# Optimization experiments

Hardware: AMD Instinct MI355X
Metric: run time of the kernel (lower is better)

## Reference

```python
import jax, jax.numpy as jnp
import numpy as np

T, B, H, V = 128, 32, 1024, 32000


def setup_inputs() -> dict:
    key = jax.random.key(0)
    ks = jax.random.split(key, 8)
    scale = 1.0 / np.sqrt(H)
    return {
        "input": jax.random.normal(ks[0], (T, B, H), dtype=jnp.float32),
        "hidden": jnp.zeros((B, H), dtype=jnp.float32),
        "w_ic": jax.random.uniform(ks[1], (H, H), jnp.float32, -scale, scale),
        "w_ix": jax.random.uniform(ks[2], (H, H), jnp.float32, -scale, scale),
        "w_fc": jax.random.uniform(ks[3], (H, H), jnp.float32, -scale, scale),
        "w_fx": jax.random.uniform(ks[4], (H, H), jnp.float32, -scale, scale),
        "b_i": jnp.zeros((H,), dtype=jnp.float32),
        "b_f": jnp.zeros((H,), dtype=jnp.float32),
        "W_out": jax.random.uniform(ks[5], (V, H), jnp.float32, -scale, scale),
        "b_out": jnp.zeros((V,), dtype=jnp.float32),
    }


def reference(input, hidden, w_ic, w_ix, w_fc, w_fx, b_i, b_f, W_out, b_out):
    # Precompute input projections for all timesteps: [T, B, H]
    ix = jnp.einsum("tbh,kh->tbk", input, w_ix)
    fx = jnp.einsum("tbh,kh->tbk", input, w_fx)

    def step(c, xs):
        ix_t, fx_t, x_t = xs
        i_t = jax.nn.sigmoid(c @ w_ic.T + b_i + ix_t)
        f_t = jax.nn.sigmoid(c @ w_fc.T + b_f + fx_t)
        c_new = i_t * x_t + f_t * c  # RAN gated-additive update
        return c_new, c_new

    hidden_final, outputs = jax.lax.scan(step, hidden, (ix, fx, input))
    logits = jnp.einsum("tbh,vh->tbv", outputs, W_out) + b_out
    log_probs = jax.nn.log_softmax(logits, axis=-1)
    return log_probs, hidden_final
```

## Files before the change

kernel.cpp:

```cpp
#include <hip/hip_runtime.h>

typedef __attribute__((ext_vector_type(4))) float f32x4;
typedef __attribute__((ext_vector_type(8))) short bf16x8;
typedef __attribute__((ext_vector_type(4))) unsigned u32x4;

#define T_DIM 128
#define B_DIM 32
#define H_DIM 1024
#define V_DIM 32000
#define MROWS 4096
#define NBLK 64
#define PUBSTEP 32768
#define WSTRIDE 1028
#define GBK 32

__device__ __forceinline__ ushort f2bf(float f){
  union { float f; unsigned u; } x; x.f = f;
  unsigned u = x.u;
  unsigned r = (u + 0x7fffu + ((u >> 16) & 1u)) >> 16;
  return (ushort)r;
}
__device__ __forceinline__ float bf2f(ushort h){
  union { unsigned u; float f; } x; x.u = ((unsigned)h) << 16;
  return x.f;
}

__device__ __forceinline__ void async_copy16(void* lds, const void* g){
  __builtin_amdgcn_global_load_lds((const __attribute__((address_space(1))) void*)g,
                                   (__attribute__((address_space(3))) void*)lds, 16, 0, 0);
}

__global__ void cast_bf16_kernel(const float* __restrict__ s, ushort* __restrict__ d, int n4){
  int stride = gridDim.x * blockDim.x;
  for (int i = blockIdx.x*blockDim.x + threadIdx.x; i < n4; i += stride){
    float4 v = ((const float4*)s)[i];
    ushort4 o = make_ushort4(f2bf(v.x), f2bf(v.y), f2bf(v.z), f2bf(v.w));
    ((ushort4*)d)[i] = o;
  }
}

__global__ void cast_split_kernel(const float* __restrict__ s, ushort* __restrict__ dh,
                                  ushort* __restrict__ dl, int n4){
  int stride = gridDim.x * blockDim.x;
  for (int i = blockIdx.x*blockDim.x + threadIdx.x; i < n4; i += stride){
    float4 v = ((const float4*)s)[i];
    ushort4 h = make_ushort4(f2bf(v.x), f2bf(v.y), f2bf(v.z), f2bf(v.w));
    ushort4 l = make_ushort4(f2bf(v.x - bf2f(h.x)), f2bf(v.y - bf2f(h.y)),
                             f2bf(v.z - bf2f(h.z)), f2bf(v.w - bf2f(h.w)));
    ((ushort4*)dh)[i] = h;
    ((ushort4*)dl)[i] = l;
  }
}

__global__ __launch_bounds__(256) void gemm_bt_plain(
    const ushort* __restrict__ A, const ushort* __restrict__ B,
    float* __restrict__ C, int N, int K, int NTN)
{
  __shared__ ushort lA[128*32];
  __shared__ ushort lB[128*32];
  int tid = threadIdx.x;
  int lane = tid & 63, wid = tid >> 6;
  int tm = blockIdx.x / NTN, tn = blockIdx.x % NTN;
  int row0 = tm << 7, col0 = tn << 7;

  f32x4 acc[4][4] = {};

  auto stage = [&](const ushort* __restrict__ g, ushort* l, int r0, int k0){
    int c = wid << 1;
    const ushort* s0 = g + (size_t)(r0 + (c<<4) + (lane>>2))*K + k0 + ((lane&3)<<3);
    async_copy16(l + (c<<9), s0);
    async_copy16(l + ((c+1)<<9), s0 + (size_t)16*K);
  };

  int nk = K >> 5;
  stage(A, lA, row0, 0);
  stage(B, lB, col0, 0);
  int wm = (wid >> 1) << 6, wn = (wid & 1) << 6;
  int kg = (lane >> 4) << 3;
  int ar = lane & 15;

  for (int kt = 0; kt < nk; ++kt){
    __syncthreads();
    bf16x8 af[4], bfr[4];
    #pragma unroll
    for (int mi = 0; mi < 4; ++mi) af[mi]  = *(const bf16x8*)&lA[(wm + mi*16 + ar)*32 + kg];
    #pragma unroll
    for (int ni = 0; ni < 4; ++ni) bfr[ni] = *(const bf16x8*)&lB[(wn + ni*16 + ar)*32 + kg];
    #pragma unroll
    for (int mi = 0; mi < 4; ++mi)
      #pragma unroll
      for (int ni = 0; ni < 4; ++ni)
        acc[mi][ni] = __builtin_amdgcn_mfma_f32_16x16x32_bf16(af[mi], bfr[ni], acc[mi][ni], 0, 0, 0);
    if (kt + 1 < nk){
      __syncthreads();
      stage(A, lA, row0, (kt+1) << 5);
      stage(B, lB, col0, (kt+1) << 5);
    }
  }

  int rr = (lane >> 4) << 2;
  #pragma unroll
  for (int mi = 0; mi < 4; ++mi)
    #pragma unroll
    for (int ni = 0; ni < 4; ++ni){
      int r  = row0 + wm + mi*16 + rr;
      int cc = col0 + wn + ni*16 + ar;
      #pragma unroll
      for (int q = 0; q < 4; ++q)
        C[(size_t)(r + q) * N + cc] = acc[mi][ni][q];
    }
}

__global__ __launch_bounds__(512) void gemm256(
    const ushort* __restrict__ A, const ushort* __restrict__ B,
    float* __restrict__ C, const float* __restrict__ bias,
    float* __restrict__ pmax, float* __restrict__ psum)
{
  __shared__ ushort lA[4][256*GBK];
  __shared__ ushort lB[4][256*GBK];
  __shared__ float redm[2][4][128], reds[2][4][128];

  const int K = 1024, N = V_DIM, NTN = 125, NT = 32;
  int tid = threadIdx.x, lane = tid & 63, wid = tid >> 6;
  int wm = wid >> 2, wn = wid & 3;
  int bid = blockIdx.x;
  int xcd = bid & 7, id = bid >> 3;
  int tm = (xcd << 1) | (id & 1);
  int tn = id >> 1;
  int row0 = tm << 8, col0 = tn << 8;
  int ar = lane & 15, kg = (lane >> 4) << 3;

  auto STAGE = [&](int slot, int kt){
    int k0 = kt << 5;
    #pragma unroll
    for (int j = 0; j < 2; ++j){
      int u = j*512 + tid;
      int r = u >> 2, p = u & 3;
      int g = p ^ ((r >> 1) & 3);
      int rA = row0 + r, k = k0 + (g << 3);
      const ushort* sA = A + ((size_t)(rA>>5)<<15) + ((size_t)(k>>4)<<9) + ((rA&31)<<4) + (k&15);
      async_copy16(&lA[slot][u<<3], sA);
    }
    #pragma unroll
    for (int j = 0; j < 2; ++j){
      int u = j*512 + tid;
      int r = u >> 2, p = u & 3;
      int g = p ^ ((r >> 1) & 3);
      const ushort* sB = B + (size_t)(col0 + r)*K + k0 + (g << 3);
      async_copy16(&lB[slot][u<<3], sB);
    }
  };

  f32x4 acc[8][4] = {};

  STAGE(0, 0);
  STAGE(1, 1);
  int gk = kg >> 3;
  for (int t = 0; t < NT; ++t){
    if (t + 2 < NT) STAGE((t+2) & 3, t+2);
    if (t + 2 < NT)      asm volatile("s_waitcnt vmcnt(8)" ::: "memory");
    else if (t + 1 < NT) asm volatile("s_waitcnt vmcnt(4)" ::: "memory");
    else                 asm volatile("s_waitcnt vmcnt(0)" ::: "memory");
    __builtin_amdgcn_s_barrier();
    __builtin_amdgcn_sched_barrier(0);
    const ushort* bufA = lA[t & 3];
    const ushort* bufB = lB[t & 3];
    bf16x8 a[8], b[4];
    #pragma unroll
    for (int fr = 0; fr < 8; ++fr){
      int row = wm*128 + fr*16 + ar;
      int phys = gk ^ ((row >> 1) & 3);
      a[fr] = *(const bf16x8*)&bufA[row*GBK + (phys << 3)];
    }
    #pragma unroll
    for (int fc = 0; fc < 4; ++fc){
      int row = wn*64 + fc*16 + ar;
      int phys = gk ^ ((row >> 1) & 3);
      b[fc] = *(const bf16x8*)&bufB[row*GBK + (phys << 3)];
    }
    __builtin_amdgcn_s_setprio(1);
    #pragma unroll
    for (int fr = 0; fr < 8; ++fr)
      #pragma unroll
      for (int fc = 0; fc < 4; ++fc)
        acc[fr][fc] = __builtin_amdgcn_mfma_f32_16x16x32_bf16(a[fr], b[fc], acc[fr][fc], 0, 0, 0);
    __builtin_amdgcn_s_setprio(0);
    __builtin_amdgcn_sched_barrier(0);
  }

  float bb4[4];
  #pragma unroll
  for (int fc = 0; fc < 4; ++fc) bb4[fc] = bias[col0 + wn*64 + fc*16 + ar];
  #pragma unroll
  for (int fr = 0; fr < 8; ++fr){
    #pragma unroll
    for (int q = 0; q < 4; ++q){
      int rl = fr*16 + (lane>>4)*4 + q;
      int r = row0 + wm*128 + rl;
      float vals[4];
      #pragma unroll
      for (int fc = 0; fc < 4; ++fc){
        vals[fc] = acc[fr][fc][q] + bb4[fc];
        C[(size_t)r * N + col0 + wn*64 + fc*16 + ar] = vals[fc];
      }
      float m = fmaxf(fmaxf(vals[0], vals[1]), fmaxf(vals[2], vals[3]));
      #pragma unroll
      for (int o = 1; o < 16; o <<= 1) m = fmaxf(m, __shfl_xor(m, o));
      float s = expf(vals[0]-m) + expf(vals[1]-m) + expf(vals[2]-m) + expf(vals[3]-m);
      #pragma unroll
      for (int o = 1; o < 16; o <<= 1) s += __shfl_xor(s, o);
      if (ar == 0){ redm[wm][wn][rl] = m; reds[wm][wn][rl] = s; }
    }
  }
  __syncthreads();
  if (tid < 256){
    int wm2 = tid >> 7, rl = tid & 127;
    float m0 = redm[wm2][0][rl], m1 = redm[wm2][1][rl];
    float m2 = redm[wm2][2][rl], m3 = redm[wm2][3][rl];
    float M = fmaxf(fmaxf(m0, m1), fmaxf(m2, m3));
    float S = reds[wm2][0][rl]*expf(m0-M) + reds[wm2][1][rl]*expf(m1-M)
            + reds[wm2][2][rl]*expf(m2-M) + reds[wm2][3][rl]*expf(m3-M);
    int r = row0 + wm2*128 + rl;
    pmax[(size_t)r*NTN + tn] = M;
    psum[(size_t)r*NTN + tn] = S;
  }
}

__global__ __launch_bounds__(512) void ran_all(
    unsigned* __restrict__ pub, ushort* __restrict__ cst,
    const float* __restrict__ hiddenf,
    const ushort* __restrict__ wh, const ushort* __restrict__ wl,
    const float* __restrict__ b_i, const float* __restrict__ b_f,
    const float* __restrict__ ixfx, const float* __restrict__ x_all,
    float* __restrict__ hid_final)
{
  __shared__ ushort lWh[32*WSTRIDE];
  __shared__ ushort lWl[32*WSTRIDE];
  __shared__ f32x4 part[4][2][2][64];
  __shared__ float gsm[2*32*17];
  __shared__ float cfl[32][17];

  int tid = threadIdx.x, lane = tid & 63, wid = tid >> 6;
  int kq = wid & 3, mh = wid >> 2;
  int rgate = wid & 1, rmh = (wid >> 1) & 1;
  int bid = blockIdx.x;
  int nb = bid << 4;
  int ar = lane & 15, kg = (lane >> 4) << 3;
  int um = tid >> 4, uk = tid & 15;

  #pragma unroll
  for (int u = 0; u < 8; ++u){
    int unit = u*512 + tid;
    int r = unit >> 7, off = (unit & 127) << 3;
    int g = r >> 4, c = r & 15;
    size_t gsrc = (size_t)((g<<10) + nb + c) * H_DIM + off;
    *(bf16x8*)&lWh[r*WSTRIDE + off] = *(const bf16x8*)&wh[gsrc];
    *(bf16x8*)&lWl[r*WSTRIDE + off] = *(const bf16x8*)&wl[gsrc];
  }
  cfl[um][uk] = hiddenf[(um<<10) + nb + uk];
  float bb = (rgate ? b_f : b_i)[nb + ar];
  const ushort* b0h = &lWh[(     ar)*WSTRIDE + (kq<<8) + kg];
  const ushort* b0l = &lWl[(     ar)*WSTRIDE + (kq<<8) + kg];
  const ushort* b1h = &lWh[(16 + ar)*WSTRIDE + (kq<<8) + kg];
  const ushort* b1l = &lWl[(16 + ar)*WSTRIDE + (kq<<8) + kg];
  int abase = (kq<<13) + ((kg>>4)<<9) + (((mh<<4) + ar)<<4) + (kg & 8);
  __syncthreads();

  for (int t = 0; t < T_DIM; ++t){
    float xq1 = x_all[((size_t)t<<15) + (um<<10) + nb + uk];
    float pix[4];
    if (wid < 4){
      const float* ix_t = ixfx + ((size_t)t<<16);
      #pragma unroll
      for (int q = 0; q < 4; ++q){
        int m = (rmh<<4) + ((lane>>4)<<2) + q;
        pix[q] = ix_t[m*2048 + (rgate<<10) + nb + ar];
      }
    }

    const unsigned* ps = pub + ((size_t)t << 15) + abase;
    unsigned expt = (unsigned)(t + 1) << 16;
    u32x4 w0[8], w1[8];
    int tries = 0;
    while (1){
      #pragma unroll
      for (int f = 0; f < 8; ++f){
        const unsigned* p = ps + (f << 10);
        asm volatile("global_load_dwordx4 %0, %2, off sc0 sc1\n\t"
                     "global_load_dwordx4 %1, %2, off offset:16 sc0 sc1"
                     : "=&v"(w0[f]), "=&v"(w1[f]) : "v"(p));
      }
      asm volatile("s_waitcnt vmcnt(0)" ::: "memory");
      __builtin_amdgcn_sched_barrier(0);
      unsigned bad = 0;
      #pragma unroll
      for (int f = 0; f < 8; ++f){
        bad |= (w0[f][0]^expt)|(w0[f][1]^expt)|(w0[f][2]^expt)|(w0[f][3]^expt)
             | (w1[f][0]^expt)|(w1[f][1]^expt)|(w1[f][2]^expt)|(w1[f][3]^expt);
      }
      if (__ballot((bad & 0xFFFF0000u) != 0) == 0ull) break;
      if (++tries > (1<<15)) break;
    }

    f32x4 g0h = {}, g0l = {}, g1h = {}, g1l = {};
    #pragma unroll
    for (int f = 0; f < 8; ++f){
      union { unsigned u[4]; bf16x8 v; } cv;
      cv.u[0] = (w0[f][0] & 0xFFFFu) | (w0[f][1] << 16);
      cv.u[1] = (w0[f][2] & 0xFFFFu) | (w0[f][3] << 16);
      cv.u[2] = (w1[f][0] & 0xFFFFu) | (w1[f][1] << 16);
      cv.u[3] = (w1[f][2] & 0xFFFFu) | (w1[f][3] << 16);
      int ob = f << 5;
      bf16x8 v0h = *(const bf16x8*)&b0h[ob];
      bf16x8 v0l = *(const bf16x8*)&b0l[ob];
      bf16x8 v1h = *(const bf16x8*)&b1h[ob];
      bf16x8 v1l = *(const bf16x8*)&b1l[ob];
      g0h = __builtin_amdgcn_mfma_f32_16x16x32_bf16(cv.v, v0h, g0h, 0, 0, 0);
      g0l = __builtin_amdgcn_mfma_f32_16x16x32_bf16(cv.v, v0l, g0l, 0, 0, 0);
      g1h = __builtin_amdgcn_mfma_f32_16x16x32_bf16(cv.v, v1h, g1h, 0, 0, 0);
      g1l = __builtin_amdgcn_mfma_f32_16x16x32_bf16(cv.v, v1l, g1l, 0, 0, 0);
    }
    part[kq][mh][0][lane] = g0h + g0l;
    part[kq][mh][1][lane] = g1h + g1l;
    __syncthreads();

    if (wid < 4){
      f32x4 sum = part[0][rmh][rgate][lane] + part[1][rmh][rgate][lane]
                + part[2][rmh][rgate][lane] + part[3][rmh][rgate][lane];
      #pragma unroll
      for (int q = 0; q < 4; ++q){
        int m = (rmh<<4) + ((lane>>4)<<2) + q;
        float pre = sum[q] + bb + pix[q];
        gsm[((rgate<<5) + m)*17 + ar] = 1.f / (1.f + expf(-pre));
      }
    }
    __syncthreads();

    {
      float iv = gsm[um*17 + uk];
      float fv = gsm[(32+um)*17 + uk];
      float cv2 = cfl[um][uk];
      float cn = iv * xq1 + fv * cv2;
      cfl[um][uk] = cn;
      ushort hb = f2bf(cn);
      unsigned word = ((unsigned)(t + 2) << 16) | (unsigned)hb;
      __hip_atomic_store(&pub[((size_t)(t+1) << 15) + (bid << 9) + tid], word,
                         __ATOMIC_RELAXED, __HIP_MEMORY_SCOPE_AGENT);
      cst[((size_t)t << 15) + (bid << 9) + tid] = hb;
      if (t == T_DIM-1) hid_final[(um<<10) + nb + uk] = cn;
    }
    __syncthreads();
  }
}

__global__ void init_c_kernel(const float* __restrict__ hidden, unsigned* __restrict__ pub){
  int i = blockIdx.x * blockDim.x + threadIdx.x;
  float v = hidden[i];
  int m = i >> 10, col = i & 1023;
  pub[((col>>4)<<9) + (m<<4) + (col&15)] = (1u << 16) | (unsigned)f2bf(v);
}

__global__ __launch_bounds__(256) void subf_kernel(float* __restrict__ logits,
                                                   const float* __restrict__ pmax,
                                                   const float* __restrict__ psum){
  __shared__ float sl;
  size_t row = blockIdx.x >> 1;
  int half = blockIdx.x & 1;
  int tid = threadIdx.x;
  if (tid < 64){
    float m = -1e30f, s = 0.f;
    for (int i = tid; i < 125; i += 64){
      float mi = pmax[row*125 + i], si = psum[row*125 + i];
      float M = fmaxf(m, mi);
      s = s*expf(m - M) + si*expf(mi - M);
      m = M;
    }
    #pragma unroll
    for (int o = 32; o; o >>= 1){
      float m2 = __shfl_xor(m, o), s2 = __shfl_xor(s, o);
      float M = fmaxf(m, m2);
      s = s*expf(m - M) + s2*expf(m2 - M);
      m = M;
    }
    if (tid == 0) sl = m + logf(s);
  }
  __syncthreads();
  float l = sl;
  float4* p4 = (float4*)(logits + row * (size_t)V_DIM);
  int beg = half * 4000, end = beg + 4000;
  for (int i = beg + tid; i < end; i += 256){
    float4 v = p4[i];
    v.x -= l; v.y -= l; v.z -= l; v.w -= l;
    p4[i] = v;
  }
}

extern "C" void kernel_launch(void* const* d_in, const int* in_sizes, int n_in,
                              void* d_out, int out_size, void* d_ws, size_t ws_size,
                              hipStream_t stream)
{
  const float* input  = (const float*)d_in[0];
  const float* hidden = (const float*)d_in[1];
  const float* w_ic   = (const float*)d_in[2];
  const float* w_ix   = (const float*)d_in[3];
  const float* w_fc   = (const float*)d_in[4];
  const float* w_fx   = (const float*)d_in[5];
  const float* b_i    = (const float*)d_in[6];
  const float* b_f    = (const float*)d_in[7];
  const float* W_out  = (const float*)d_in[8];
  const float* b_out  = (const float*)d_in[9];
  float* out = (float*)d_out;

  char* ws = (char*)d_ws;
  ushort* wout_bf = (ushort*)(ws + 0);
  ushort* in_hi   = (ushort*)(ws + 65536000);
  ushort* wx      = (ushort*)(ws + 73924608);
  ushort* wc_hi   = (ushort*)(ws + 90701824);
  ushort* wc_lo   = (ushort*)(ws + 94896128);
  unsigned* pub   = (unsigned*)(ws + 65536000);
  ushort* cstate  = (ushort*)(ws + 82444288);
  float*  pmax    = (float*)(ws + 94896128);
  float*  psum    = (float*)(ws + 99090432);
  float*  ixfx    = out;

  cast_bf16_kernel<<<2048,256,0,stream>>>(W_out, wout_bf, V_DIM*H_DIM/4);
  cast_bf16_kernel<<<1024,256,0,stream>>>(input, in_hi, MROWS*H_DIM/4);
  cast_bf16_kernel<<<256,256,0,stream>>>(w_ix, wx,             H_DIM*H_DIM/4);
  cast_bf16_kernel<<<256,256,0,stream>>>(w_fx, wx+H_DIM*H_DIM, H_DIM*H_DIM/4);
  cast_split_kernel<<<256,256,0,stream>>>(w_ic, wc_hi,             wc_lo,             H_DIM*H_DIM/4);
  cast_split_kernel<<<256,256,0,stream>>>(w_fc, wc_hi+H_DIM*H_DIM, wc_lo+H_DIM*H_DIM, H_DIM*H_DIM/4);

  gemm_bt_plain<<<32*16,256,0,stream>>>(in_hi, wx, ixfx, 2048, H_DIM, 16);

  hipMemsetAsync(pub, 0, (size_t)129 * PUBSTEP * 4, stream);
  init_c_kernel<<<128,256,0,stream>>>(hidden, pub);

  ran_all<<<NBLK,512,0,stream>>>(pub, cstate, hidden, wc_hi, wc_lo, b_i, b_f,
                                 ixfx, input, out + (size_t)MROWS*V_DIM);

  gemm256<<<2000,512,0,stream>>>(cstate, wout_bf, out, b_out, pmax, psum);
  subf_kernel<<<2*MROWS,256,0,stream>>>(out, pmax, psum);
}
```

Before: 1.867 ms.

## Replace input-projection GEMM with 256x256 multi-buffered swizzled MFMA kernel

Swaps the 128x128 single-buffered input projection GEMM for a 256x256 tile kernel with a 4-slot LDS ring and prefetch two K-steps ahead. LDS tiles use an XOR swizzle, and waits use explicit vmcnt counts instead of full barriers. The aim is to hide global load latency and raise MFMA reuse for the 4096x2048x1024 projection. The trade-off is fewer blocks (128 on a GPU with many CUs), more LDS per block and higher register pressure from 32 accumulator tiles.

Result: no change. 1.863 ms (-0.3%).

```diff
diff --git a/kernel.cpp b/kernel.cpp
--- a/kernel.cpp
+++ b/kernel.cpp
@@ -52,63 +52,86 @@
   }
 }
 
-__global__ __launch_bounds__(256) void gemm_bt_plain(
-    const ushort* __restrict__ A, const ushort* __restrict__ B,
-    float* __restrict__ C, int N, int K, int NTN)
+__global__ __launch_bounds__(512) void gemm256_ix(
+    const ushort* __restrict__ A, const ushort* __restrict__ B, float* __restrict__ C)
 {
-  __shared__ ushort lA[128*32];
-  __shared__ ushort lB[128*32];
-  int tid = threadIdx.x;
-  int lane = tid & 63, wid = tid >> 6;
-  int tm = blockIdx.x / NTN, tn = blockIdx.x % NTN;
-  int row0 = tm << 7, col0 = tn << 7;
-
-  f32x4 acc[4][4] = {};
-
-  auto stage = [&](const ushort* __restrict__ g, ushort* l, int r0, int k0){
-    int c = wid << 1;
-    const ushort* s0 = g + (size_t)(r0 + (c<<4) + (lane>>2))*K + k0 + ((lane&3)<<3);
-    async_copy16(l + (c<<9), s0);
-    async_copy16(l + ((c+1)<<9), s0 + (size_t)16*K);
+  __shared__ ushort lA[4][256*GBK];
+  __shared__ ushort lB[4][256*GBK];
+
+  const int K = 1024, N = 2048, NT = 32;
+  int tid = threadIdx.x, lane = tid & 63, wid = tid >> 6;
+  int wm = wid >> 2, wn = wid & 3;
+  int tn = blockIdx.x & 7, tm = blockIdx.x >> 3;
+  int row0 = tm << 8, col0 = tn << 8;
+  int ar = lane & 15, kg = (lane >> 4) << 3;
+
+  auto STAGE = [&](int slot, int kt){
+    int k0 = kt << 5;
+    #pragma unroll
+    for (int j = 0; j < 2; ++j){
+      int u = j*512 + tid;
+      int r = u >> 2, p = u & 3;
+      int g = p ^ ((r >> 1) & 3);
+      const ushort* sA = A + (size_t)(row0 + r)*K + k0 + (g << 3);
+      async_copy16(&lA[slot][u<<3], sA);
+    }
+    #pragma unroll
+    for (int j = 0; j < 2; ++j){
+      int u = j*512 + tid;
+      int r = u >> 2, p = u & 3;
+      int g = p ^ ((r >> 1) & 3);
+      const ushort* sB = B + (size_t)(col0 + r)*K + k0 + (g << 3);
+      async_copy16(&lB[slot][u<<3], sB);
+    }
   };
 
-  int nk = K >> 5;
-  stage(A, lA, row0, 0);
-  stage(B, lB, col0, 0);
-  int wm = (wid >> 1) << 6, wn = (wid & 1) << 6;
-  int kg = (lane >> 4) << 3;
-  int ar = lane & 15;
-
-  for (int kt = 0; kt < nk; ++kt){
-    __syncthreads();
-    bf16x8 af[4], bfr[4];
-    #pragma unroll
-    for (int mi = 0; mi < 4; ++mi) af[mi]  = *(const bf16x8*)&lA[(wm + mi*16 + ar)*32 + kg];
-    #pragma unroll
-    for (int ni = 0; ni < 4; ++ni) bfr[ni] = *(const bf16x8*)&lB[(wn + ni*16 + ar)*32 + kg];
-    #pragma unroll
-    for (int mi = 0; mi < 4; ++mi)
-      #pragma unroll
-      for (int ni = 0; ni < 4; ++ni)
-        acc[mi][ni] = __builtin_amdgcn_mfma_f32_16x16x32_bf16(af[mi], bfr[ni], acc[mi][ni], 0, 0, 0);
-    if (kt + 1 < nk){
-      __syncthreads();
-      stage(A, lA, row0, (kt+1) << 5);
-      stage(B, lB, col0, (kt+1) << 5);
-    }
-  }
-
-  int rr = (lane >> 4) << 2;
+  f32x4 acc[8][4] = {};
+
+  STAGE(0, 0);
+  STAGE(1, 1);
+  int gk = kg >> 3;
+  for (int t = 0; t < NT; ++t){
+    if (t + 2 < NT) STAGE((t+2) & 3, t+2);
+    if (t + 2 < NT)      asm volatile("s_waitcnt vmcnt(8)" ::: "memory");
+    else if (t + 1 < NT) asm volatile("s_waitcnt vmcnt(4)" ::: "memory");
+    else                 asm volatile("s_waitcnt vmcnt(0)" ::: "memory");
+    __builtin_amdgcn_s_barrier();
+    __builtin_amdgcn_sched_barrier(0);
+    const ushort* bufA = lA[t & 3];
+    const ushort* bufB = lB[t & 3];
+    bf16x8 a[8], b[4];
+    #pragma unroll
+    for (int fr = 0; fr < 8; ++fr){
+      int row = wm*128 + fr*16 + ar;
+      int phys = gk ^ ((row >> 1) & 3);
+      a[fr] = *(const bf16x8*)&bufA[row*GBK + (phys << 3)];
+    }
+    #pragma unroll
+    for (int fc = 0; fc < 4; ++fc){
+      int row = wn*64 + fc*16 + ar;
+      int phys = gk ^ ((row >> 1) & 3);
+      b[fc] = *(const bf16x8*)&bufB[row*GBK + (phys << 3)];
+    }
+    __builtin_amdgcn_s_setprio(1);
+    #pragma unroll
+    for (int fr = 0; fr < 8; ++fr)
+      #pragma unroll
+      for (int fc = 0; fc < 4; ++fc)
+        acc[fr][fc] = __builtin_amdgcn_mfma_f32_16x16x32_bf16(a[fr], b[fc], acc[fr][fc], 0, 0, 0);
+    __builtin_amdgcn_s_setprio(0);
+    __builtin_amdgcn_sched_barrier(0);
+  }
+
   #pragma unroll
-  for (int mi = 0; mi < 4; ++mi)
-    #pragma unroll
-    for (int ni = 0; ni < 4; ++ni){
-      int r  = row0 + wm + mi*16 + rr;
-      int cc = col0 + wn + ni*16 + ar;
-      #pragma unroll
-      for (int q = 0; q < 4; ++q)
-        C[(size_t)(r + q) * N + cc] = acc[mi][ni][q];
-    }
+  for (int fr = 0; fr < 8; ++fr){
+    #pragma unroll
+    for (int q = 0; q < 4; ++q){
+      int r = row0 + wm*128 + fr*16 + (lane>>4)*4 + q;
+      #pragma unroll
+      for (int fc = 0; fc < 4; ++fc)
+        C[(size_t)r * N + col0 + wn*64 + fc*16 + ar] = acc[fr][fc][q];
+    }
+  }
 }
 
 __global__ __launch_bounds__(512) void gemm256(
@@ -430,7 +453,7 @@
   cast_split_kernel<<<256,256,0,stream>>>(w_ic, wc_hi,             wc_lo,             H_DIM*H_DIM/4);
   cast_split_kernel<<<256,256,0,stream>>>(w_fc, wc_hi+H_DIM*H_DIM, wc_lo+H_DIM*H_DIM, H_DIM*H_DIM/4);
 
-  gemm_bt_plain<<<32*16,256,0,stream>>>(in_hi, wx, ixfx, 2048, H_DIM, 16);
+  gemm256_ix<<<128,512,0,stream>>>(in_hi, wx, ixfx);
 
   hipMemsetAsync(pub, 0, (size_t)129 * PUBSTEP * 4, stream);
   init_c_kernel<<<128,256,0,stream>>>(hidden, pub);
```
